# Performance work log

Measured on AMD Instinct MI355X. Metric: run time of the kernel, lower is better.

Reference implementation:

```python
import jax, jax.numpy as jnp
import numpy as np

N, CIN, COUT, T, V, K = 32, 64, 64, 1024, 25, 3
EPS = 1e-5  # BatchNorm2d default eps


def setup_inputs() -> dict:
    key = jax.random.key(0)
    ks = jax.random.split(key, 7)
    x = jax.random.normal(ks[0], (N, CIN, T, V), jnp.float32)
    W = jax.random.normal(ks[1], (K * COUT, CIN), jnp.float32) * 0.05  # 1x1 conv weight (squeezed)
    b = jax.random.normal(ks[2], (K * COUT,), jnp.float32) * 0.01
    A = jax.random.uniform(ks[3], (K, V, V), jnp.float32) * 0.1       # fixed adjacency buffer
    PA = jax.random.normal(ks[4], (K, V, V), jnp.float32) * 0.01      # learned adjacency offset
    gamma = jnp.ones((COUT,), jnp.float32)
    beta = jnp.zeros((COUT,), jnp.float32)
    return {"x": x, "W": W, "b": b, "A": A, "PA": PA, "gamma": gamma, "beta": beta}


def reference(x, W, b, A, PA, gamma, beta):
    n, c, t, v = x.shape
    # 1x1 conv: [n,c,t,v] x [K*COUT, c] -> [n, K*COUT, t, v]
    y = jnp.einsum('nctv,oc->notv', x, W) + b[None, :, None, None]
    y = y.reshape(n, K, COUT, t, v)
    Afull = A + PA
    # multi-subset spatial graph aggregation over joints v -> w
    agg = jnp.einsum('nkctv,kvw->nctw', y, Afull)
    # BatchNorm2d (training mode: biased batch stats over N,T,V per channel)
    mu = jnp.mean(agg, axis=(0, 2, 3), keepdims=True)
    var = jnp.var(agg, axis=(0, 2, 3), keepdims=True)
    normed = gamma[None, :, None, None] * (agg - mu) * jax.lax.rsqrt(var + EPS) + beta[None, :, None, None]
    # residual is Identity (in_channels == out_channels), then ReLU
    return jax.nn.relu(normed + x)
```

## Files before the change

kernel.cpp:

```cpp
#include <hip/hip_runtime.h>

#define N_    32
#define CIN_  64
#define COUT_ 64
#define T_    1024
#define V_    25
#define K_    3
#define TT_   2
#define EPSV  1e-5f

#define WS_BIAS2  2112
#define WS_SUM    9856
#define WS_SQ     10368
#define WS_SCALE  10880
#define WS_SHIFT  10944
#define WS_A2F    11008
#define WS_W2F    12288

typedef __attribute__((ext_vector_type(4))) float f32x4;
typedef __attribute__((ext_vector_type(8))) short short8;

__device__ __forceinline__ unsigned short f_to_bf16u(float f) {
    unsigned int b = __float_as_uint(f);
    b += 0x7fffu + ((b >> 16) & 1u);
    return (unsigned short)(b >> 16);
}

__global__ void gcn_prep(const float* __restrict__ A, const float* __restrict__ PA,
                         const float* __restrict__ b, const float* __restrict__ W,
                         float* ws) {
    __shared__ float cs[K_ * V_];
    const int tid = threadIdx.x;
    const int blk = blockIdx.x;

    if (blk == 0) {
        if (tid < K_ * V_) {
            int k = tid / V_, w = tid % V_;
            float s = 0.f;
            for (int v = 0; v < V_; ++v) {
                int idx = (k * V_ + v) * V_ + w;
                s += A[idx] + PA[idx];
            }
            cs[tid] = s;
        }
        for (int f = tid; f < 1024; f += 256) ws[WS_SUM + f] = 0.f;
        __syncthreads();
        for (int f = tid; f < COUT_ * V_; f += 256) {
            int c = f / V_, w = f - (f / V_) * V_;
            float s = 0.f;
            for (int k = 0; k < K_; ++k) s += b[k * COUT_ + c] * cs[k * V_ + w];
            ws[WS_BIAS2 + f] = s;
        }
    } else if (blk == 1) {
        unsigned short* a2 = (unsigned short*)(ws + WS_A2F);
        for (int f = tid; f < 5 * 64 * 8; f += 256) {
            int j  = f & 7;
            int l  = (f >> 3) & 63;
            int nt = f >> 9;
            int col = nt * 16 + (l & 15);
            int v   = (l >> 4) * 8 + j;
            float val = 0.f;
            if (col < 75 && v < V_) {
                int k = col / 25, w = col - (col / 25) * 25;
                int idx = (k * V_ + v) * V_ + w;
                val = A[idx] + PA[idx];
            }
            a2[f] = f_to_bf16u(val);
        }
    } else {
        unsigned short* w2 = (unsigned short*)(ws + WS_W2F);
        int lo = (blk - 2) * 6144;
        for (int f = lo + tid; f < lo + 6144; f += 256) {
            int j = f & 7;
            int l = (f >> 3) & 63;
            int g = f >> 9;
            int kci = (g % 6) * 32 + (l >> 4) * 8 + j;
            int c   = (g / 6) * 16 + (l & 15);
            int k = kci >> 6, ci = kci & 63;
            w2[f] = f_to_bf16u(W[(k * 64 + c) * 64 + ci]);
        }
    }
}

__global__ __launch_bounds__(256, 4)
void gcn_main(const float* __restrict__ x, float* __restrict__ ws,
              float* __restrict__ out) {
    __shared__ __align__(16) unsigned char smem[35840];
    unsigned short* xs16 = (unsigned short*)smem;
    unsigned short* xa16 = (unsigned short*)(smem + 10240);

    const int tid = threadIdx.x;
    const int bid = blockIdx.x;
    const int n   = bid >> 9;
    const int tc  = bid & 511;
    const int l   = tid & 63;
    const int wv  = tid >> 6;
    const int llo = l & 15;
    const int lhi = l >> 4;

    {
        unsigned int* xu = (unsigned int*)xs16;
        #pragma unroll
        for (int i = 0; i < 10; ++i) xu[i * 256 + tid] = 0u;
    }
    __syncthreads();

    const float2* xg = (const float2*)x;
    for (int f = tid; f < CIN_ * 25; f += 256) {
        int ci = f / 25;
        int j  = f - ci * 25;
        float2 g = xg[(size_t)(n * CIN_ + ci) * 12800 + tc * 25 + j];
        int flat = 2 * j;
        int t = (flat >= 25) ? 1 : 0;
        int v = flat - 25 * t;
        xs16[(t * 64 + ci) * 40 + v] = f_to_bf16u(g.x);
        int v2 = v + 1, t2 = t;
        if (v2 == 25) { v2 = 0; t2 = 1; }
        xs16[(t2 * 64 + ci) * 40 + v2] = f_to_bf16u(g.y);
    }
    __syncthreads();

    {
        const unsigned short* a2g = (const unsigned short*)(ws + WS_A2F);
        short8 a2f[5];
        #pragma unroll
        for (int nt = 0; nt < 5; ++nt)
            a2f[nt] = *(const short8*)(a2g + (nt * 64 + l) * 8);

        #pragma unroll
        for (int q = 0; q < 2; ++q) {
            int mt = wv * 2 + q;
            short8 xf = *(const short8*)(xs16 + (mt * 16 + llo) * 40 + lhi * 8);
            int rb = mt * 16 + lhi * 4;
            int t  = rb >> 6;
            int ci = rb & 63;
            #pragma unroll
            for (int nt = 0; nt < 5; ++nt) {
                f32x4 z = {0.f, 0.f, 0.f, 0.f};
                f32x4 acc = __builtin_amdgcn_mfma_f32_16x16x32_bf16(xf, a2f[nt], z, 0, 0, 0);
                int col = nt * 16 + llo;
                if (col < 75) {
                    int k = (col >= 50) ? 2 : ((col >= 25) ? 1 : 0);
                    int w = col - k * 25;
                    unsigned int lo = (unsigned int)f_to_bf16u(acc[0]) |
                                      ((unsigned int)f_to_bf16u(acc[1]) << 16);
                    unsigned int hi = (unsigned int)f_to_bf16u(acc[2]) |
                                      ((unsigned int)f_to_bf16u(acc[3]) << 16);
                    uint2 pk; pk.x = lo; pk.y = hi;
                    *(uint2*)(xa16 + (t * 25 + w) * 200 + k * 64 + ci) = pk;
                }
            }
        }
    }
    __syncthreads();

    {
        const unsigned short* w2g = (const unsigned short*)(ws + WS_W2F);
        short8 w2f[6];
        #pragma unroll
        for (int kk = 0; kk < 6; ++kk)
            w2f[kk] = *(const short8*)(w2g + ((wv * 6 + kk) * 64 + l) * 8);

        const int c = wv * 16 + llo;
        const size_t obase = ((size_t)(n * COUT_ + c)) * 25600 + (size_t)tc * 50;
        float lsum = 0.f, lsq = 0.f;

        #pragma unroll
        for (int mt = 0; mt < 4; ++mt) {
            f32x4 acc = {0.f, 0.f, 0.f, 0.f};
            #pragma unroll
            for (int kk = 0; kk < 6; ++kk) {
                short8 a = *(const short8*)(xa16 + (mt * 16 + llo) * 200 + kk * 32 + lhi * 8);
                acc = __builtin_amdgcn_mfma_f32_16x16x32_bf16(a, w2f[kk], acc, 0, 0, 0);
            }
            int rbase = mt * 16 + lhi * 4;
            #pragma unroll
            for (int i = 0; i < 4; ++i) {
                int r = rbase + i;
                if (r < 50) {
                    int t2 = (r >= 25) ? 1 : 0;
                    int w2 = r - 25 * t2;
                    float v = acc[i] + ws[WS_BIAS2 + c * 25 + w2];
                    out[obase + r] = v;
                    lsum += v;
                    lsq = fmaf(v, v, lsq);
                }
            }
        }
        lsum += __shfl_xor(lsum, 16);
        lsum += __shfl_xor(lsum, 32);
        lsq  += __shfl_xor(lsq, 16);
        lsq  += __shfl_xor(lsq, 32);
        if (l < 16) {
            int slot = bid & 7;
            atomicAdd(&ws[WS_SUM + slot * 64 + c], lsum);
            atomicAdd(&ws[WS_SQ  + slot * 64 + c], lsq);
        }
    }
}

__global__ void gcn_stats(float* ws, const float* __restrict__ gamma,
                          const float* __restrict__ beta) {
    int c = threadIdx.x;
    if (c < COUT_) {
        float s = 0.f, q = 0.f;
        #pragma unroll
        for (int slot = 0; slot < 8; ++slot) {
            s += ws[WS_SUM + slot * 64 + c];
            q += ws[WS_SQ  + slot * 64 + c];
        }
        const float cnt = (float)(N_ * T_ * V_);
        float mu  = s / cnt;
        float var = q / cnt - mu * mu;
        float rs  = rsqrtf(var + EPSV);
        float sc  = gamma[c] * rs;
        ws[WS_SCALE + c] = sc;
        ws[WS_SHIFT + c] = fmaf(-mu, sc, beta[c]);
    }
}

__global__ __launch_bounds__(256)
void gcn_finish(const float* __restrict__ x, const float* __restrict__ ws,
                float* __restrict__ out) {
    int bid = blockIdx.x;
    int c = bid & 63;
    float sc = ws[WS_SCALE + c];
    float sh = ws[WS_SHIFT + c];
    size_t base4 = (size_t)bid * 6400;
    const float4* x4 = (const float4*)x;
    float4* o4 = (float4*)out;
    #pragma unroll 2
    for (int it = 0; it < 25; ++it) {
        size_t i = base4 + it * 256 + threadIdx.x;
        float4 a  = o4[i];
        float4 xv = x4[i];
        a.x = fmaxf(0.f, fmaf(a.x, sc, sh) + xv.x);
        a.y = fmaxf(0.f, fmaf(a.y, sc, sh) + xv.y);
        a.z = fmaxf(0.f, fmaf(a.z, sc, sh) + xv.z);
        a.w = fmaxf(0.f, fmaf(a.w, sc, sh) + xv.w);
        o4[i] = a;
    }
}

extern "C" void kernel_launch(void* const* d_in, const int* in_sizes, int n_in,
                              void* d_out, int out_size, void* d_ws, size_t ws_size,
                              hipStream_t stream) {
    (void)in_sizes; (void)n_in; (void)out_size; (void)ws_size;
    const float* x     = (const float*)d_in[0];
    const float* W     = (const float*)d_in[1];
    const float* b     = (const float*)d_in[2];
    const float* A     = (const float*)d_in[3];
    const float* PA    = (const float*)d_in[4];
    const float* gamma = (const float*)d_in[5];
    const float* beta  = (const float*)d_in[6];
    float* out = (float*)d_out;
    float* ws  = (float*)d_ws;

    gcn_prep<<<4, 256, 0, stream>>>(A, PA, b, W, ws);
    gcn_main<<<N_ * (T_ / TT_), 256, 0, stream>>>(x, ws, out);
    gcn_stats<<<1, 64, 0, stream>>>(ws, gamma, beta);
    gcn_finish<<<N_ * COUT_, 256, 0, stream>>>(x, ws, out);
}
```

Measured before the change: 647.2 us.

## Make gcn_main persistent with register-prefetched x loads and hoisted weights

```diff
diff --git a/kernel.cpp b/kernel.cpp
--- a/kernel.cpp
+++ b/kernel.cpp
@@ -6,8 +6,11 @@
 #define T_    1024
 #define V_    25
 #define K_    3
-#define TT_   2
 #define EPSV  1e-5f
+
+#define CHUNKS_TOTAL   16384
+#define GRID_MAIN      1024
+#define ITERS          (CHUNKS_TOTAL / GRID_MAIN)
 
 #define WS_BIAS2  2112
 #define WS_SUM    9856
@@ -18,12 +21,22 @@
 #define WS_W2F    12288
 
 typedef __attribute__((ext_vector_type(4))) float f32x4;
+typedef __attribute__((ext_vector_type(4), aligned(4))) float f32x4u;
 typedef __attribute__((ext_vector_type(8))) short short8;
 
 __device__ __forceinline__ unsigned short f_to_bf16u(float f) {
     unsigned int b = __float_as_uint(f);
     b += 0x7fffu + ((b >> 16) & 1u);
     return (unsigned short)(b >> 16);
+}
+
+__device__ __forceinline__ short8 pack8(const f32x4& a, const f32x4& b) {
+    short8 r;
+    r[0] = (short)f_to_bf16u(a[0]); r[1] = (short)f_to_bf16u(a[1]);
+    r[2] = (short)f_to_bf16u(a[2]); r[3] = (short)f_to_bf16u(a[3]);
+    r[4] = (short)f_to_bf16u(b[0]); r[5] = (short)f_to_bf16u(b[1]);
+    r[6] = (short)f_to_bf16u(b[2]); r[7] = (short)f_to_bf16u(b[3]);
+    return r;
 }
 
 __global__ void gcn_prep(const float* __restrict__ A, const float* __restrict__ PA,
@@ -85,55 +98,82 @@
 __global__ __launch_bounds__(256, 4)
 void gcn_main(const float* __restrict__ x, float* __restrict__ ws,
               float* __restrict__ out) {
-    __shared__ __align__(16) unsigned char smem[35840];
-    unsigned short* xs16 = (unsigned short*)smem;
-    unsigned short* xa16 = (unsigned short*)(smem + 10240);
+    __shared__ __align__(16) unsigned short xa16[50 * 200];
 
     const int tid = threadIdx.x;
-    const int bid = blockIdx.x;
-    const int n   = bid >> 9;
-    const int tc  = bid & 511;
     const int l   = tid & 63;
     const int wv  = tid >> 6;
     const int llo = l & 15;
     const int lhi = l >> 4;
 
+    const unsigned short* a2g = (const unsigned short*)(ws + WS_A2F);
+    short8 a2f[5];
+    #pragma unroll
+    for (int nt = 0; nt < 5; ++nt)
+        a2f[nt] = *(const short8*)(a2g + (nt * 64 + l) * 8);
+
+    const unsigned short* w2g = (const unsigned short*)(ws + WS_W2F);
+    short8 w2f[6];
+    #pragma unroll
+    for (int kk = 0; kk < 6; ++kk)
+        w2f[kk] = *(const short8*)(w2g + ((wv * 6 + kk) * 64 + l) * 8);
+
+    float breg[4][4];
+    #pragma unroll
+    for (int mt = 0; mt < 4; ++mt) {
+        int r = mt * 16 + llo;
+        int w2i = (r < 50) ? ((r >= 25) ? r - 25 : r) : 0;
+        #pragma unroll
+        for (int i = 0; i < 4; ++i)
+            breg[mt][i] = ws[WS_BIAS2 + (wv * 16 + lhi * 4 + i) * 25 + w2i];
+    }
+
+    float ls[4] = {0.f, 0.f, 0.f, 0.f};
+    float lq[4] = {0.f, 0.f, 0.f, 0.f};
+
+    int mtq[2], tq[2], ciq[2];
+    #pragma unroll
+    for (int q = 0; q < 2; ++q) {
+        mtq[q] = wv * 2 + q;
+        tq[q]  = mtq[q] >> 2;
+        ciq[q] = (mtq[q] * 16 + llo) & 63;
+    }
+
+    const size_t cbase_off = (size_t)(wv * 16 + lhi * 4) * 25600 + llo;
+
+    const int chunk0 = blockIdx.x * ITERS;
+
+    f32x4 xr[2][2];
     {
-        unsigned int* xu = (unsigned int*)xs16;
-        #pragma unroll
-        for (int i = 0; i < 10; ++i) xu[i * 256 + tid] = 0u;
-    }
-    __syncthreads();
-
-    const float2* xg = (const float2*)x;
-    for (int f = tid; f < CIN_ * 25; f += 256) {
-        int ci = f / 25;
-        int j  = f - ci * 25;
-        float2 g = xg[(size_t)(n * CIN_ + ci) * 12800 + tc * 25 + j];
-        int flat = 2 * j;
-        int t = (flat >= 25) ? 1 : 0;
-        int v = flat - 25 * t;
-        xs16[(t * 64 + ci) * 40 + v] = f_to_bf16u(g.x);
-        int v2 = v + 1, t2 = t;
-        if (v2 == 25) { v2 = 0; t2 = 1; }
-        xs16[(t2 * 64 + ci) * 40 + v2] = f_to_bf16u(g.y);
-    }
-    __syncthreads();
-
-    {
-        const unsigned short* a2g = (const unsigned short*)(ws + WS_A2F);
-        short8 a2f[5];
-        #pragma unroll
-        for (int nt = 0; nt < 5; ++nt)
-            a2f[nt] = *(const short8*)(a2g + (nt * 64 + l) * 8);
-
+        int n = chunk0 >> 9, tc = chunk0 & 511;
         #pragma unroll
         for (int q = 0; q < 2; ++q) {
-            int mt = wv * 2 + q;
-            short8 xf = *(const short8*)(xs16 + (mt * 16 + llo) * 40 + lhi * 8);
-            int rb = mt * 16 + lhi * 4;
-            int t  = rb >> 6;
-            int ci = rb & 63;
+            const float* src = x + (size_t)(n * 64 + ciq[q]) * 25600
+                                 + (size_t)(tc * 2 + tq[q]) * 25 + lhi * 8;
+            if (lhi < 3) {
+                xr[q][0] = *(const f32x4u*)src;
+                xr[q][1] = *(const f32x4u*)(src + 4);
+            } else {
+                f32x4 z = {src[0], 0.f, 0.f, 0.f};
+                xr[q][0] = z;
+                f32x4 zz = {0.f, 0.f, 0.f, 0.f};
+                xr[q][1] = zz;
+            }
+        }
+    }
+
+    #pragma unroll 1
+    for (int it = 0; it < ITERS; ++it) {
+        const int chunk = chunk0 + it;
+        const int n  = chunk >> 9;
+        const int tc = chunk & 511;
+
+        #pragma unroll
+        for (int q = 0; q < 2; ++q) {
+            short8 xf = pack8(xr[q][0], xr[q][1]);
+            int rb  = mtq[q] * 16 + lhi * 4;
+            int t   = rb >> 6;
+            int ci4 = rb & 63;
             #pragma unroll
             for (int nt = 0; nt < 5; ++nt) {
                 f32x4 z = {0.f, 0.f, 0.f, 0.f};
@@ -147,54 +187,69 @@
                     unsigned int hi = (unsigned int)f_to_bf16u(acc[2]) |
                                       ((unsigned int)f_to_bf16u(acc[3]) << 16);
                     uint2 pk; pk.x = lo; pk.y = hi;
-                    *(uint2*)(xa16 + (t * 25 + w) * 200 + k * 64 + ci) = pk;
+                    *(uint2*)(xa16 + (t * 25 + w) * 200 + k * 64 + ci4) = pk;
                 }
             }
         }
-    }
-    __syncthreads();
-
-    {
-        const unsigned short* w2g = (const unsigned short*)(ws + WS_W2F);
-        short8 w2f[6];
-        #pragma unroll
-        for (int kk = 0; kk < 6; ++kk)
-            w2f[kk] = *(const short8*)(w2g + ((wv * 6 + kk) * 64 + l) * 8);
-
-        const int c = wv * 16 + llo;
-        const size_t obase = ((size_t)(n * COUT_ + c)) * 25600 + (size_t)tc * 50;
-        float lsum = 0.f, lsq = 0.f;
-
-        #pragma unroll
-        for (int mt = 0; mt < 4; ++mt) {
+        __syncthreads();
+
+        if (it + 1 < ITERS) {
+            int nn = (chunk + 1) >> 9, ntc = (chunk + 1) & 511;
+            #pragma unroll
+            for (int q = 0; q < 2; ++q) {
+                const float* src = x + (size_t)(nn * 64 + ciq[q]) * 25600
+                                     + (size_t)(ntc * 2 + tq[q]) * 25 + lhi * 8;
+                if (lhi < 3) {
+                    xr[q][0] = *(const f32x4u*)src;
+                    xr[q][1] = *(const f32x4u*)(src + 4);
+                } else {
+                    f32x4 z = {src[0], 0.f, 0.f, 0.f};
+                    xr[q][0] = z;
+                    f32x4 zz = {0.f, 0.f, 0.f, 0.f};
+                    xr[q][1] = zz;
+                }
+            }
+        }
+
+        const size_t iterbase = (size_t)n * 64 * 25600 + (size_t)tc * 50 + cbase_off;
+        #pragma unroll
+        for (int mt2 = 0; mt2 < 4; ++mt2) {
+            int rr  = mt2 * 16 + llo;
+            int row = (rr < 50) ? rr : 0;
             f32x4 acc = {0.f, 0.f, 0.f, 0.f};
             #pragma unroll
             for (int kk = 0; kk < 6; ++kk) {
-                short8 a = *(const short8*)(xa16 + (mt * 16 + llo) * 200 + kk * 32 + lhi * 8);
-                acc = __builtin_amdgcn_mfma_f32_16x16x32_bf16(a, w2f[kk], acc, 0, 0, 0);
-            }
-            int rbase = mt * 16 + lhi * 4;
-            #pragma unroll
-            for (int i = 0; i < 4; ++i) {
-                int r = rbase + i;
-                if (r < 50) {
-                    int t2 = (r >= 25) ? 1 : 0;
-                    int w2 = r - 25 * t2;
-                    float v = acc[i] + ws[WS_BIAS2 + c * 25 + w2];
-                    out[obase + r] = v;
-                    lsum += v;
-                    lsq = fmaf(v, v, lsq);
+                short8 bxa = *(const short8*)(xa16 + row * 200 + kk * 32 + lhi * 8);
+                acc = __builtin_amdgcn_mfma_f32_16x16x32_bf16(w2f[kk], bxa, acc, 0, 0, 0);
+            }
+            if (rr < 50) {
+                #pragma unroll
+                for (int i = 0; i < 4; ++i) {
+                    float v = acc[i] + breg[mt2][i];
+                    out[iterbase + (size_t)i * 25600 + mt2 * 16] = v;
+                    ls[i] += v;
+                    lq[i] = fmaf(v, v, lq[i]);
                 }
             }
         }
-        lsum += __shfl_xor(lsum, 16);
-        lsum += __shfl_xor(lsum, 32);
-        lsq  += __shfl_xor(lsq, 16);
-        lsq  += __shfl_xor(lsq, 32);
-        if (l < 16) {
-            int slot = bid & 7;
-            atomicAdd(&ws[WS_SUM + slot * 64 + c], lsum);
-            atomicAdd(&ws[WS_SQ  + slot * 64 + c], lsq);
+        __syncthreads();
+    }
+
+    #pragma unroll
+    for (int i = 0; i < 4; ++i) {
+        #pragma unroll
+        for (int m = 1; m <= 8; m <<= 1) {
+            ls[i] += __shfl_xor(ls[i], m);
+            lq[i] += __shfl_xor(lq[i], m);
+        }
+    }
+    if (llo == 0) {
+        int slot = blockIdx.x & 7;
+        int cb = wv * 16 + lhi * 4;
+        #pragma unroll
+        for (int i = 0; i < 4; ++i) {
+            atomicAdd(&ws[WS_SUM + slot * 64 + cb + i], ls[i]);
+            atomicAdd(&ws[WS_SQ  + slot * 64 + cb + i], lq[i]);
         }
     }
 }
@@ -257,7 +312,7 @@
     float* ws  = (float*)d_ws;
 
     gcn_prep<<<4, 256, 0, stream>>>(A, PA, b, W, ws);
-    gcn_main<<<N_ * (T_ / TT_), 256, 0, stream>>>(x, ws, out);
+    gcn_main<<<GRID_MAIN, 256, 0, stream>>>(x, ws, out);
     gcn_stats<<<1, 64, 0, stream>>>(ws, gamma, beta);
     gcn_finish<<<N_ * COUT_, 256, 0, stream>>>(x, ws, out);
 }
```

New measurement: 557.0 us. 1.16x faster.
